# Optimization experiments

Hardware: AMD Instinct MI355X
Metric: run time of the kernel (lower is better)

## Reference

```python
import jax, jax.numpy as jnp
import numpy as np

VOCAB, E, H = 32000, 256, 256
B, T = 64, 2048


def setup_inputs() -> dict:
    key = jax.random.key(0)
    ks = jax.random.split(key, 6)
    X = jax.random.randint(ks[0], (B, T), 0, VOCAB)
    emb = jax.random.normal(ks[1], (VOCAB, E), dtype=jnp.float32)
    W_qrnn = jax.random.normal(ks[2], (E, 3 * H), dtype=jnp.float32) / np.sqrt(E)
    b_qrnn = jnp.zeros((3 * H,), dtype=jnp.float32)
    c0 = jax.random.normal(ks[3], (B, H), dtype=jnp.float32)
    W_out = jax.random.normal(ks[4], (H, 1), dtype=jnp.float32) / np.sqrt(H)
    b_out = jnp.zeros((1,), dtype=jnp.float32)
    return {"X": X, "emb": emb, "W_qrnn": W_qrnn, "b_qrnn": b_qrnn,
            "c0": c0, "W_out": W_out, "b_out": b_out}


def reference(X, emb, W_qrnn, b_qrnn, c0, W_out, b_out):
    # Embedding lookup: [B,T] -> [B,T,E]; permute to seq-major [T,B,E]
    x = jnp.transpose(emb[X], (1, 0, 2))
    # QRNN window=1 gate projection: all timesteps in one GEMM, [T,B,3H]
    g = jnp.einsum('tbe,ef->tbf', x, W_qrnn) + b_qrnn
    z, f, o = jnp.split(g, 3, axis=-1)
    z = jnp.tanh(z)
    f = jax.nn.sigmoid(f)
    o = jax.nn.sigmoid(o)

    # fo-pooling recurrence: c_t = f_t * c_{t-1} + (1 - f_t) * z_t
    def step(c, zf):
        z_t, f_t = zf
        c = f_t * c + (1.0 - f_t) * z_t
        return c, c

    _, cs = jax.lax.scan(step, c0, (z, f))  # cs: [T,B,H]
    h = o * cs                              # h_t = o_t * c_t
    hn = h[-1]                              # last timestep, [B,H]
    return hn @ W_out + b_out               # [B,1]
```

## Files before the change

### kernel.cpp

```cpp
#include <hip/hip_runtime.h>
#include <hip/hip_bf16.h>
#include <math.h>

#define EDIM 256
#define HDIM 256
#define BDIM 64
#define TDIM 2048
#define NC   64
#define TC   32
#define CPB  4

typedef __attribute__((ext_vector_type(8)))  short  short8;
typedef __attribute__((ext_vector_type(4)))  float  floatx4;
typedef __attribute__((ext_vector_type(4)))  unsigned int uintx4;

__device__ __forceinline__ unsigned short f2bf(float f) {
    unsigned int u = __float_as_uint(f);
    u += 0x7FFFu + ((u >> 16) & 1u);
    return (unsigned short)(u >> 16);
}
__device__ __forceinline__ unsigned int pk2(float a, float b) {
    return (unsigned int)f2bf(a) | ((unsigned int)f2bf(b) << 16);
}
__device__ __forceinline__ float sigm(float x) {
    return __builtin_amdgcn_rcpf(1.f + __expf(-x));
}
__device__ __forceinline__ float tanh_fast(float x) {
    return fmaf(-2.f, __builtin_amdgcn_rcpf(1.f + __expf(2.f * x)), 1.f);
}

__global__ __launch_bounds__(256) void qrnn_pack(
    const float* __restrict__ Wq, const float* __restrict__ emb,
    unsigned short* __restrict__ Wp, unsigned short* __restrict__ ebf)
{
    const int bx = blockIdx.x;
    if (bx < 256) {
        const int nt = (bx >> 3) & 7;
        const int hg = bx >> 6;
        const int ks = bx & 7;
        const int t = threadIdx.x;
        const int lane = t >> 2, pj = t & 3;
        const int col = lane & 15, q = lane >> 4;
        const int h = hg * 64 + (nt & 3) * 16 + col;
        const int c = (nt < 4) ? h : (HDIM + h);
        const int k = ks * 32 + q * 8 + pj * 2;
        unsigned int v = pk2(Wq[k * (3 * HDIM) + c], Wq[(k + 1) * (3 * HDIM) + c]);
        *(unsigned int*)(Wp + (size_t)bx * 512 + lane * 8 + pj * 2) = v;
    } else {
        size_t i = ((size_t)(bx - 256) * 256 + threadIdx.x) * 8;
        floatx4 a = *(const floatx4*)(emb + i);
        floatx4 b = *(const floatx4*)(emb + i + 4);
        uintx4 o = {pk2(a.x, a.y), pk2(a.z, a.w), pk2(b.x, b.y), pk2(b.z, b.w)};
        *(uintx4*)(ebf + i) = o;
    }
}

template<bool EMBBF>
__global__ __launch_bounds__(256, 2) void qrnn_mfma(
    const int* __restrict__ X, const float* __restrict__ emb,
    const unsigned short* __restrict__ ebf, const unsigned short* __restrict__ Wp,
    const float* __restrict__ bq, float* __restrict__ wsA, float* __restrict__ wsB)
{
    __shared__ __align__(16) short Bsh[32768];

    const int tid = threadIdx.x;
    const int cgi = blockIdx.x, bg = blockIdx.y, hg = blockIdx.z;
    const int lane = tid & 63, w = tid >> 6;
    const int col = lane & 15, q = lane >> 4;

    const unsigned short* wpb = Wp + (size_t)hg * 32768;
#pragma unroll
    for (int i = 0; i < 16; ++i) {
        const int ch = w * 16 + i;
        __builtin_amdgcn_global_load_lds(
            (const __attribute__((address_space(1))) unsigned int*)(wpb + ch * 512 + lane * 8),
            (__attribute__((address_space(3))) unsigned int*)(Bsh + ch * 512),
            16, 0, 0);
    }

    const int b0 = bg * 8 + 2 * w;
    int xid[CPB][4];
#pragma unroll
    for (int c = 0; c < CPB; ++c)
#pragma unroll
        for (int mt = 0; mt < 4; ++mt)
            xid[c][mt] = X[(b0 + (mt >> 1)) * TDIM + (cgi * CPB + c) * TC + (mt & 1) * 16 + col];

    const int hbase = hg * 64;
    float bz[4], bff[4];
#pragma unroll
    for (int nt = 0; nt < 4; ++nt) {
        bz[nt]  = bq[hbase + nt * 16 + col];
        bff[nt] = bq[HDIM + hbase + nt * 16 + col];
    }

    short8 abuf[3][4];
    auto fetchA = [&](int c, int ks, int slot) {
#pragma unroll
        for (int mt = 0; mt < 4; ++mt) {
            if constexpr (EMBBF) {
                abuf[slot][mt] = *(const short8*)(ebf + (size_t)xid[c][mt] * EDIM + q * 8 + ks * 32);
            } else {
                const float* ap = emb + (size_t)xid[c][mt] * EDIM + q * 8 + ks * 32;
                floatx4 f0 = *(const floatx4*)ap;
                floatx4 f1 = *(const floatx4*)(ap + 4);
                uintx4 p = {pk2(f0.x, f0.y), pk2(f0.z, f0.w),
                            pk2(f1.x, f1.y), pk2(f1.z, f1.w)};
                abuf[slot][mt] = *(short8*)&p;
            }
        }
    };

    floatx4 acc[4][8];
#pragma unroll
    for (int mt = 0; mt < 4; ++mt)
#pragma unroll
        for (int nt = 0; nt < 8; ++nt) acc[mt][nt] = (floatx4){0.f, 0.f, 0.f, 0.f};

    fetchA(0, 0, 0);
    fetchA(0, 1, 1);
    __syncthreads();

#pragma unroll
    for (int c = 0; c < CPB; ++c) {
#pragma unroll
        for (int ks = 0; ks < 8; ++ks) {
            const int s = c * 8 + ks;
            if (s + 2 < CPB * 8)
                fetchA((s + 2) >> 3, (s + 2) & 7, (s + 2) % 3);
            const int sl = s % 3;
#pragma unroll
            for (int nh = 0; nh < 2; ++nh) {
                short8 bf[4];
#pragma unroll
                for (int j = 0; j < 4; ++j)
                    bf[j] = *(const short8*)(Bsh + ((nh * 4 + j) * 8 + ks) * 512 + lane * 8);
#pragma unroll
                for (int j = 0; j < 4; ++j)
#pragma unroll
                    for (int mt = 0; mt < 4; ++mt)
                        acc[mt][nh * 4 + j] = __builtin_amdgcn_mfma_f32_16x16x32_bf16(
                            abuf[sl][mt], bf[j], acc[mt][nh * 4 + j], 0, 0, 0);
            }
        }

        const int cc = cgi * CPB + c;
        const size_t r0 = ((size_t)cc * BDIM + b0) * HDIM + hbase + lane;
#pragma unroll
        for (int nt = 0; nt < 4; ++nt) {
            float Aseg[4], Bseg[4];
#pragma unroll
            for (int mt = 0; mt < 4; ++mt) {
                float Ac = 1.f, Bc = 0.f;
#pragma unroll
                for (int j = 0; j < 4; ++j) {
                    float z = tanh_fast(acc[mt][nt][j] + bz[nt]);
                    float f = sigm(acc[mt][nt + 4][j] + bff[nt]);
                    Ac = f * Ac;
                    Bc = fmaf(f, Bc - z, z);
                }
                Aseg[mt] = Ac; Bseg[mt] = Bc;
            }
#pragma unroll
            for (int st = 0; st < 2; ++st) {
                const int msk = 16 << st;
                const bool self_earlier = ((q >> st) & 1) == 0;
#pragma unroll
                for (int mt = 0; mt < 4; ++mt) {
                    float Ap = __shfl_xor(Aseg[mt], msk, 64);
                    float Bp = __shfl_xor(Bseg[mt], msk, 64);
                    Bseg[mt] = self_earlier ? fmaf(Ap, Bseg[mt], Bp)
                                            : fmaf(Aseg[mt], Bp, Bseg[mt]);
                    Aseg[mt] = Aseg[mt] * Ap;
                }
            }
            if (q == nt) {
                wsA[r0]        = Aseg[0] * Aseg[1];
                wsB[r0]        = fmaf(Aseg[1], Bseg[0], Bseg[1]);
                wsA[r0 + HDIM] = Aseg[2] * Aseg[3];
                wsB[r0 + HDIM] = fmaf(Aseg[3], Bseg[2], Bseg[3]);
            }
        }

#pragma unroll
        for (int mt = 0; mt < 4; ++mt)
#pragma unroll
            for (int nt = 0; nt < 8; ++nt) acc[mt][nt] = (floatx4){0.f, 0.f, 0.f, 0.f};
    }
}

__global__ __launch_bounds__(256) void qrnn_combine(
    const float* __restrict__ wsA, const float* __restrict__ wsB,
    const float* __restrict__ c0, const int* __restrict__ X,
    const float* __restrict__ emb, const float* __restrict__ Wq,
    const float* __restrict__ bq, const float* __restrict__ Wout,
    const float* __restrict__ bout, float* __restrict__ out)
{
    const int b = blockIdx.x;
    const int h = threadIdx.x;

    float c = c0[b * HDIM + h];
    for (int c8 = 0; c8 < NC; c8 += 8) {
        float a[8], bb[8];
#pragma unroll
        for (int i = 0; i < 8; ++i) {
            size_t base = ((size_t)(c8 + i) * BDIM + b) * HDIM + h;
            a[i]  = wsA[base];
            bb[i] = wsB[base];
        }
#pragma unroll
        for (int i = 0; i < 8; ++i) c = fmaf(a[i], c, bb[i]);
    }

    __shared__ float xs[EDIM];
    int idx = X[b * TDIM + (TDIM - 1)];
    xs[h] = emb[(size_t)idx * EDIM + h];
    __syncthreads();

    float acc = 0.f;
#pragma unroll 16
    for (int e = 0; e < EDIM; ++e)
        acc = fmaf(xs[e], Wq[e * (3 * HDIM) + 2 * HDIM + h], acc);

    float o  = 1.f / (1.f + expf(-(acc + bq[2 * HDIM + h])));
    float hn = o * c;

    __shared__ float red[HDIM];
    red[h] = hn * Wout[h];
    __syncthreads();
    for (int s = HDIM / 2; s > 0; s >>= 1) {
        if (h < s) red[h] += red[h + s];
        __syncthreads();
    }
    if (h == 0) out[b] = red[0] + bout[0];
}

extern "C" void kernel_launch(void* const* d_in, const int* in_sizes, int n_in,
                              void* d_out, int out_size, void* d_ws, size_t ws_size,
                              hipStream_t stream) {
    const int*   X    = (const int*)d_in[0];
    const float* emb  = (const float*)d_in[1];
    const float* Wq   = (const float*)d_in[2];
    const float* bq   = (const float*)d_in[3];
    const float* c0   = (const float*)d_in[4];
    const float* Wout = (const float*)d_in[5];
    const float* bout = (const float*)d_in[6];
    float* out = (float*)d_out;

    float* wsA = (float*)d_ws;
    float* wsB = wsA + (size_t)NC * BDIM * HDIM;
    unsigned short* Wp  = (unsigned short*)(wsB + (size_t)NC * BDIM * HDIM);
    unsigned short* ebf = Wp + (size_t)256 * 512;

    const size_t need_full = (size_t)2 * NC * BDIM * HDIM * 4
                           + (size_t)256 * 512 * 2
                           + (size_t)32000 * EDIM * 2;
    const bool full = ws_size >= need_full;

    const int emb_blocks = (32000 * EDIM / 8) / 256;
    qrnn_pack<<<256 + (full ? emb_blocks : 0), 256, 0, stream>>>(Wq, emb, Wp, ebf);

    dim3 g(NC / CPB, BDIM / 8, HDIM / 64);
    if (full) qrnn_mfma<true ><<<g, 256, 0, stream>>>(X, emb, ebf, Wp, bq, wsA, wsB);
    else      qrnn_mfma<false><<<g, 256, 0, stream>>>(X, emb, ebf, Wp, bq, wsA, wsB);

    qrnn_combine<<<BDIM, 256, 0, stream>>>(wsA, wsB, c0, X, emb, Wq, bq, Wout, bout, out);
}
```

Baseline: 158.3 us.

## Remap MFMA grid to 1D with XCD-aware block order and branchless stores

Switches the 3D grid to a 1D grid of 512 blocks whose index is decoded so that the blocks sharing an XCD (consecutive modulo 8) cover the four h-groups of the same token/batch tile, improving L2 reuse of gathered embedding rows. Precomputes 32-bit embedding offsets per token to cut 64-bit address arithmetic. Replaces the per-nt conditional global stores with register selection followed by a single unconditional store set. Adds some register pressure and select instructions.

```diff
diff --git a/kernel.cpp b/kernel.cpp
--- a/kernel.cpp
+++ b/kernel.cpp
@@ -64,7 +64,11 @@
     __shared__ __align__(16) short Bsh[32768];
 
     const int tid = threadIdx.x;
-    const int cgi = blockIdx.x, bg = blockIdx.y, hg = blockIdx.z;
+    const int bid = blockIdx.x;
+    const int hg  = (bid >> 3) & 3;
+    const int g   = ((bid >> 5) << 3) + (bid & 7);
+    const int cgi = g & 15, bg = g >> 4;
+
     const int lane = tid & 63, w = tid >> 6;
     const int col = lane & 15, q = lane >> 4;
 
@@ -79,12 +83,14 @@
     }
 
     const int b0 = bg * 8 + 2 * w;
-    int xid[CPB][4];
+    unsigned int voff[CPB][4];
 #pragma unroll
     for (int c = 0; c < CPB; ++c)
 #pragma unroll
-        for (int mt = 0; mt < 4; ++mt)
-            xid[c][mt] = X[(b0 + (mt >> 1)) * TDIM + (cgi * CPB + c) * TC + (mt & 1) * 16 + col];
+        for (int mt = 0; mt < 4; ++mt) {
+            int xv = X[(b0 + (mt >> 1)) * TDIM + (cgi * CPB + c) * TC + (mt & 1) * 16 + col];
+            voff[c][mt] = (unsigned int)xv * EDIM + q * 8;
+        }
 
     const int hbase = hg * 64;
     float bz[4], bff[4];
@@ -95,13 +101,14 @@
     }
 
     short8 abuf[3][4];
-    auto fetchA = [&](int c, int ks, int slot) {
+    auto fetchA = [&](int step, int slot) {
+        const int c = step >> 3, ko = (step & 7) * 32;
 #pragma unroll
         for (int mt = 0; mt < 4; ++mt) {
             if constexpr (EMBBF) {
-                abuf[slot][mt] = *(const short8*)(ebf + (size_t)xid[c][mt] * EDIM + q * 8 + ks * 32);
+                abuf[slot][mt] = *(const short8*)(ebf + voff[c][mt] + ko);
             } else {
-                const float* ap = emb + (size_t)xid[c][mt] * EDIM + q * 8 + ks * 32;
+                const float* ap = emb + voff[c][mt] + ko;
                 floatx4 f0 = *(const floatx4*)ap;
                 floatx4 f1 = *(const floatx4*)(ap + 4);
                 uintx4 p = {pk2(f0.x, f0.y), pk2(f0.z, f0.w),
@@ -117,8 +124,8 @@
 #pragma unroll
         for (int nt = 0; nt < 8; ++nt) acc[mt][nt] = (floatx4){0.f, 0.f, 0.f, 0.f};
 
-    fetchA(0, 0, 0);
-    fetchA(0, 1, 1);
+    fetchA(0, 0);
+    fetchA(1, 1);
     __syncthreads();
 
 #pragma unroll
@@ -127,7 +134,7 @@
         for (int ks = 0; ks < 8; ++ks) {
             const int s = c * 8 + ks;
             if (s + 2 < CPB * 8)
-                fetchA((s + 2) >> 3, (s + 2) & 7, (s + 2) % 3);
+                fetchA(s + 2, (s + 2) % 3);
             const int sl = s % 3;
 #pragma unroll
             for (int nh = 0; nh < 2; ++nh) {
@@ -145,7 +152,7 @@
         }
 
         const int cc = cgi * CPB + c;
-        const size_t r0 = ((size_t)cc * BDIM + b0) * HDIM + hbase + lane;
+        float Af0[4], Bf0[4], Af1[4], Bf1[4];
 #pragma unroll
         for (int nt = 0; nt < 4; ++nt) {
             float Aseg[4], Bseg[4];
@@ -174,13 +181,20 @@
                     Aseg[mt] = Aseg[mt] * Ap;
                 }
             }
-            if (q == nt) {
-                wsA[r0]        = Aseg[0] * Aseg[1];
-                wsB[r0]        = fmaf(Aseg[1], Bseg[0], Bseg[1]);
-                wsA[r0 + HDIM] = Aseg[2] * Aseg[3];
-                wsB[r0 + HDIM] = fmaf(Aseg[3], Bseg[2], Bseg[3]);
-            }
-        }
+            Af0[nt] = Aseg[0] * Aseg[1];
+            Bf0[nt] = fmaf(Aseg[1], Bseg[0], Bseg[1]);
+            Af1[nt] = Aseg[2] * Aseg[3];
+            Bf1[nt] = fmaf(Aseg[3], Bseg[2], Bseg[3]);
+        }
+
+        float As0 = (q == 0) ? Af0[0] : (q == 1) ? Af0[1] : (q == 2) ? Af0[2] : Af0[3];
+        float Bs0 = (q == 0) ? Bf0[0] : (q == 1) ? Bf0[1] : (q == 2) ? Bf0[2] : Bf0[3];
+        float As1 = (q == 0) ? Af1[0] : (q == 1) ? Af1[1] : (q == 2) ? Af1[2] : Af1[3];
+        float Bs1 = (q == 0) ? Bf1[0] : (q == 1) ? Bf1[1] : (q == 2) ? Bf1[2] : Bf1[3];
+
+        const size_t r0 = ((size_t)cc * BDIM + b0) * HDIM + hbase + lane;
+        wsA[r0] = As0;          wsB[r0] = Bs0;
+        wsA[r0 + HDIM] = As1;   wsB[r0 + HDIM] = Bs1;
 
 #pragma unroll
         for (int mt = 0; mt < 4; ++mt)
@@ -260,9 +274,8 @@
     const int emb_blocks = (32000 * EDIM / 8) / 256;
     qrnn_pack<<<256 + (full ? emb_blocks : 0), 256, 0, stream>>>(Wq, emb, Wp, ebf);
 
-    dim3 g(NC / CPB, BDIM / 8, HDIM / 64);
-    if (full) qrnn_mfma<true ><<<g, 256, 0, stream>>>(X, emb, ebf, Wp, bq, wsA, wsB);
-    else      qrnn_mfma<false><<<g, 256, 0, stream>>>(X, emb, ebf, Wp, bq, wsA, wsB);
+    if (full) qrnn_mfma<true ><<<512, 256, 0, stream>>>(X, emb, ebf, Wp, bq, wsA, wsB);
+    else      qrnn_mfma<false><<<512, 256, 0, stream>>>(X, emb, ebf, Wp, bq, wsA, wsB);
 
     qrnn_combine<<<BDIM, 256, 0, stream>>>(wsA, wsB, c0, X, emb, Wq, bq, Wout, bout, out);
 }
```

New measurement: 151.6 us. -4.2%, faster.

## Split MFMA work by hidden column per wave and swizzle block order

Applied to the files above, without the earlier changes.

Each wave now owns one 16-column slice of the z and f gates and covers all 4 batches × 2 time halves (8 M tiles), where before it covered 2 batches across all columns. This cuts LDS B-fragment reads per MFMA and the accumulator footprint, but each wave now gathers 8 embedding rows per k-step, twice as many. Blocks are launched as a 1D grid with a swizzled index so that blocks sharing the same column group run together. Token ids for the next chunk are prefetched in rolling fashion instead of all up front, and offsets switch to 32-bit arithmetic.

```diff
diff --git a/kernel.cpp b/kernel.cpp
--- a/kernel.cpp
+++ b/kernel.cpp
@@ -64,44 +64,47 @@
     __shared__ __align__(16) short Bsh[32768];
 
     const int tid = threadIdx.x;
-    const int cgi = blockIdx.x, bg = blockIdx.y, hg = blockIdx.z;
-    const int lane = tid & 63, w = tid >> 6;
+    const int bid = blockIdx.x;
+    const int hg  = (bid >> 3) & 3;
+    const int g   = ((bid >> 5) << 3) | (bid & 7);
+    const int cgi = g & 15, bg = g >> 4;
+
+    const int lane = tid & 63, nw = tid >> 6;
     const int col = lane & 15, q = lane >> 4;
 
     const unsigned short* wpb = Wp + (size_t)hg * 32768;
 #pragma unroll
     for (int i = 0; i < 16; ++i) {
-        const int ch = w * 16 + i;
+        const int ch = nw * 16 + i;
         __builtin_amdgcn_global_load_lds(
             (const __attribute__((address_space(1))) unsigned int*)(wpb + ch * 512 + lane * 8),
             (__attribute__((address_space(3))) unsigned int*)(Bsh + ch * 512),
             16, 0, 0);
     }
 
-    const int b0 = bg * 8 + 2 * w;
-    int xid[CPB][4];
-#pragma unroll
-    for (int c = 0; c < CPB; ++c)
-#pragma unroll
-        for (int mt = 0; mt < 4; ++mt)
-            xid[c][mt] = X[(b0 + (mt >> 1)) * TDIM + (cgi * CPB + c) * TC + (mt & 1) * 16 + col];
+    const int b0 = bg * 4;
+    int xc[8], xn[8];
+    auto loadX = [&](int cc, int* arr) {
+#pragma unroll
+        for (int mt = 0; mt < 8; ++mt)
+            arr[mt] = X[(b0 + (mt >> 1)) * TDIM + cc * TC + (mt & 1) * 16 + col];
+    };
+    loadX(cgi * CPB + 0, xc);
+    loadX(cgi * CPB + 1, xn);
 
     const int hbase = hg * 64;
-    float bz[4], bff[4];
-#pragma unroll
-    for (int nt = 0; nt < 4; ++nt) {
-        bz[nt]  = bq[hbase + nt * 16 + col];
-        bff[nt] = bq[HDIM + hbase + nt * 16 + col];
-    }
-
-    short8 abuf[3][4];
-    auto fetchA = [&](int c, int ks, int slot) {
-#pragma unroll
-        for (int mt = 0; mt < 4; ++mt) {
+    const float bzv = bq[hbase + nw * 16 + col];
+    const float bfv = bq[HDIM + hbase + nw * 16 + col];
+
+    short8 abuf[3][8];
+    auto fetchA = [&](const int* xa, int ks, int slot) {
+#pragma unroll
+        for (int mt = 0; mt < 8; ++mt) {
+            const unsigned int vo = (unsigned int)xa[mt] * EDIM + q * 8 + ks * 32;
             if constexpr (EMBBF) {
-                abuf[slot][mt] = *(const short8*)(ebf + (size_t)xid[c][mt] * EDIM + q * 8 + ks * 32);
+                abuf[slot][mt] = *(const short8*)(ebf + vo);
             } else {
-                const float* ap = emb + (size_t)xid[c][mt] * EDIM + q * 8 + ks * 32;
+                const float* ap = emb + vo;
                 floatx4 f0 = *(const floatx4*)ap;
                 floatx4 f1 = *(const floatx4*)(ap + 4);
                 uintx4 p = {pk2(f0.x, f0.y), pk2(f0.z, f0.w),
@@ -111,14 +114,15 @@
         }
     };
 
-    floatx4 acc[4][8];
-#pragma unroll
-    for (int mt = 0; mt < 4; ++mt)
-#pragma unroll
-        for (int nt = 0; nt < 8; ++nt) acc[mt][nt] = (floatx4){0.f, 0.f, 0.f, 0.f};
-
-    fetchA(0, 0, 0);
-    fetchA(0, 1, 1);
+    floatx4 acc[8][2];
+#pragma unroll
+    for (int mt = 0; mt < 8; ++mt) {
+        acc[mt][0] = (floatx4){0.f, 0.f, 0.f, 0.f};
+        acc[mt][1] = (floatx4){0.f, 0.f, 0.f, 0.f};
+    }
+
+    fetchA(xc, 0, 0);
+    fetchA(xc, 1, 1);
     __syncthreads();
 
 #pragma unroll
@@ -126,66 +130,68 @@
 #pragma unroll
         for (int ks = 0; ks < 8; ++ks) {
             const int s = c * 8 + ks;
-            if (s + 2 < CPB * 8)
-                fetchA((s + 2) >> 3, (s + 2) & 7, (s + 2) % 3);
+            if (s + 2 < CPB * 8) {
+                const int t = s + 2;
+                fetchA(((t >> 3) == c) ? xc : xn, t & 7, t % 3);
+            }
+            short8 bf0 = *(const short8*)(Bsh + (nw * 8 + ks) * 512 + lane * 8);
+            short8 bf1 = *(const short8*)(Bsh + ((nw + 4) * 8 + ks) * 512 + lane * 8);
             const int sl = s % 3;
 #pragma unroll
-            for (int nh = 0; nh < 2; ++nh) {
-                short8 bf[4];
-#pragma unroll
-                for (int j = 0; j < 4; ++j)
-                    bf[j] = *(const short8*)(Bsh + ((nh * 4 + j) * 8 + ks) * 512 + lane * 8);
-#pragma unroll
-                for (int j = 0; j < 4; ++j)
-#pragma unroll
-                    for (int mt = 0; mt < 4; ++mt)
-                        acc[mt][nh * 4 + j] = __builtin_amdgcn_mfma_f32_16x16x32_bf16(
-                            abuf[sl][mt], bf[j], acc[mt][nh * 4 + j], 0, 0, 0);
+            for (int mt = 0; mt < 8; ++mt) {
+                acc[mt][0] = __builtin_amdgcn_mfma_f32_16x16x32_bf16(abuf[sl][mt], bf0, acc[mt][0], 0, 0, 0);
+                acc[mt][1] = __builtin_amdgcn_mfma_f32_16x16x32_bf16(abuf[sl][mt], bf1, acc[mt][1], 0, 0, 0);
             }
         }
 
         const int cc = cgi * CPB + c;
-        const size_t r0 = ((size_t)cc * BDIM + b0) * HDIM + hbase + lane;
-#pragma unroll
-        for (int nt = 0; nt < 4; ++nt) {
-            float Aseg[4], Bseg[4];
-#pragma unroll
-            for (int mt = 0; mt < 4; ++mt) {
+#pragma unroll
+        for (int bt = 0; bt < 4; ++bt) {
+            float Aseg[2], Bseg[2];
+#pragma unroll
+            for (int th = 0; th < 2; ++th) {
                 float Ac = 1.f, Bc = 0.f;
 #pragma unroll
                 for (int j = 0; j < 4; ++j) {
-                    float z = tanh_fast(acc[mt][nt][j] + bz[nt]);
-                    float f = sigm(acc[mt][nt + 4][j] + bff[nt]);
+                    float z = tanh_fast(acc[bt * 2 + th][0][j] + bzv);
+                    float f = sigm(acc[bt * 2 + th][1][j] + bfv);
                     Ac = f * Ac;
                     Bc = fmaf(f, Bc - z, z);
                 }
-                Aseg[mt] = Ac; Bseg[mt] = Bc;
+                Aseg[th] = Ac; Bseg[th] = Bc;
             }
 #pragma unroll
             for (int st = 0; st < 2; ++st) {
                 const int msk = 16 << st;
                 const bool self_earlier = ((q >> st) & 1) == 0;
 #pragma unroll
-                for (int mt = 0; mt < 4; ++mt) {
-                    float Ap = __shfl_xor(Aseg[mt], msk, 64);
-                    float Bp = __shfl_xor(Bseg[mt], msk, 64);
-                    Bseg[mt] = self_earlier ? fmaf(Ap, Bseg[mt], Bp)
-                                            : fmaf(Aseg[mt], Bp, Bseg[mt]);
-                    Aseg[mt] = Aseg[mt] * Ap;
+                for (int th = 0; th < 2; ++th) {
+                    float Ap = __shfl_xor(Aseg[th], msk, 64);
+                    float Bp = __shfl_xor(Bseg[th], msk, 64);
+                    Bseg[th] = self_earlier ? fmaf(Ap, Bseg[th], Bp)
+                                            : fmaf(Aseg[th], Bp, Bseg[th]);
+                    Aseg[th] = Aseg[th] * Ap;
                 }
             }
-            if (q == nt) {
-                wsA[r0]        = Aseg[0] * Aseg[1];
-                wsB[r0]        = fmaf(Aseg[1], Bseg[0], Bseg[1]);
-                wsA[r0 + HDIM] = Aseg[2] * Aseg[3];
-                wsB[r0 + HDIM] = fmaf(Aseg[3], Bseg[2], Bseg[3]);
-            }
-        }
-
-#pragma unroll
-        for (int mt = 0; mt < 4; ++mt)
-#pragma unroll
-            for (int nt = 0; nt < 8; ++nt) acc[mt][nt] = (floatx4){0.f, 0.f, 0.f, 0.f};
+            const float Afin = Aseg[1] * Aseg[0];
+            const float Bfin = fmaf(Aseg[1], Bseg[0], Bseg[1]);
+            if (q == bt) {
+                const size_t r = ((size_t)cc * BDIM + b0 + bt) * HDIM + hbase + nw * 16 + col;
+                wsA[r] = Afin;
+                wsB[r] = Bfin;
+            }
+        }
+
+#pragma unroll
+        for (int mt = 0; mt < 8; ++mt) {
+            acc[mt][0] = (floatx4){0.f, 0.f, 0.f, 0.f};
+            acc[mt][1] = (floatx4){0.f, 0.f, 0.f, 0.f};
+        }
+        if (c < CPB - 1) {
+#pragma unroll
+            for (int mt = 0; mt < 8; ++mt) xc[mt] = xn[mt];
+            if (c < CPB - 2) loadX(cgi * CPB + c + 2, xn);
+        }
     }
 }
 
@@ -260,9 +266,8 @@
     const int emb_blocks = (32000 * EDIM / 8) / 256;
     qrnn_pack<<<256 + (full ? emb_blocks : 0), 256, 0, stream>>>(Wq, emb, Wp, ebf);
 
-    dim3 g(NC / CPB, BDIM / 8, HDIM / 64);
-    if (full) qrnn_mfma<true ><<<g, 256, 0, stream>>>(X, emb, ebf, Wp, bq, wsA, wsB);
-    else      qrnn_mfma<false><<<g, 256, 0, stream>>>(X, emb, ebf, Wp, bq, wsA, wsB);
+    if (full) qrnn_mfma<true ><<<1024, 256, 0, stream>>>(X, emb, ebf, Wp, bq, wsA, wsB);
+    else      qrnn_mfma<false><<<1024, 256, 0, stream>>>(X, emb, ebf, Wp, bq, wsA, wsB);
 
     qrnn_combine<<<BDIM, 256, 0, stream>>>(wsA, wsB, c0, X, emb, Wq, bq, Wout, bout, out);
 }
```

New measurement: 221.4 us. +39.9%, slower.
